# Performance work log

Hardware: AMD Instinct MI355X
Metric: run time of the kernel (lower is better)

## Reference

```python
import jax, jax.numpy as jnp
import numpy as np

NUM_TOKENS = 4096
IN_FEATURES = 4096
OUT_FEATURES = 4096
MAX_PACKED = 4


def setup_inputs() -> dict:
    key = jax.random.key(0)
    k1, k2, k3 = jax.random.split(key, 3)
    x = jax.random.normal(k1, (NUM_TOKENS, IN_FEATURES), dtype=jnp.float32)
    weight_stacked = jax.random.normal(
        k2, (MAX_PACKED, OUT_FEATURES, IN_FEATURES), dtype=jnp.float32) * 0.02
    indices = jax.random.randint(k3, (NUM_TOKENS,), 0, MAX_PACKED, dtype=jnp.int32)
    return {"x": x, "weight_stacked": weight_stacked, "indices": indices}


def reference(x, weight_stacked, indices):
    # apply_swap: outputs[t] = x[t] @ weight_stacked[indices[t]].T
    # Grouped-GEMM expressed as E dense GEMMs with masked combine
    # (E = max_packed is a small static constant).
    E = weight_stacked.shape[0]
    out = jnp.zeros((x.shape[0], weight_stacked.shape[1]), dtype=x.dtype)
    for e in range(E):
        sel = (indices == e)[:, None].astype(x.dtype)  # [T,1]
        out = out + sel * jnp.einsum('ti,oi->to', x, weight_stacked[e])
    return out
```

## Files before the change

### kernel.cpp

```cpp
#include <hip/hip_runtime.h>

#define T 4096
#define K 4096
#define O 4096
#define E 4
#define BK 64
#define MAXT128 35

typedef __attribute__((ext_vector_type(8))) short bf16x8;
typedef __attribute__((ext_vector_type(4))) float f32x4;

__device__ __forceinline__ unsigned short f2bf(float f) {
  unsigned int u = __float_as_uint(f);
  u += 0x7fffu + ((u >> 16) & 1u);
  return (unsigned short)(u >> 16);
}

__global__ void build_meta(const int* __restrict__ idx, int* __restrict__ perm,
                           int* __restrict__ meta, int4* __restrict__ t256,
                           int4* __restrict__ t128, int4* __restrict__ sched) {
  const int wave = threadIdx.x >> 6;
  const int lane = threadIdx.x & 63;
  __shared__ int s_off[E + 1];
  __shared__ int rtE[20], rtP[20], rtC[20];
  __shared__ int r_sh;
  int total = 0;
  for (int t0 = 0; t0 < T; t0 += 64)
    total += __popcll(__ballot(idx[t0 + lane] == wave));
  if (lane == 0) s_off[wave + 1] = total;
  __syncthreads();
  if (threadIdx.x == 0) {
    s_off[0] = 0;
    for (int e = 0; e < E; e++) s_off[e + 1] += s_off[e];
  }
  __syncthreads();
  int base = s_off[wave];
  const unsigned long long below = (1ull << lane) - 1ull;
  for (int t0 = 0; t0 < T; t0 += 64) {
    int e = idx[t0 + lane];
    unsigned long long m = __ballot(e == wave);
    if (e == wave) perm[base + __popcll(m & below)] = t0 + lane;
    base += __popcll(m);
  }
  if (threadIdx.x == 0) {
    int n = 0;
    for (int e = 0; e < E; e++) {
      int s = s_off[e], c = s_off[e + 1] - s;
      for (int ro = 0; ro < c; ro += 256) {
        rtE[n] = e; rtP[n] = s + ro; rtC[n] = (c - ro) < 256 ? (c - ro) : 256; n++;
      }
    }
    r_sh = n;
    meta[0] = n * 16;
    int n1 = 0;
    for (int e = 0; e < E; e++) {
      int s = s_off[e], c = s_off[e + 1] - s;
      for (int ro = 0; ro < c; ro += 128)
        t128[n1++] = make_int4(e, s + ro, (c - ro) < 128 ? (c - ro) : 128, 0);
    }
    for (; n1 < MAXT128; n1++) t128[n1] = make_int4(-1, 0, 0, 0);
  }
  __syncthreads();
  const int r = r_sh;
  for (int i = threadIdx.x; i < 16 * r; i += 256)
    t256[i] = make_int4(rtE[i >> 4], rtP[i >> 4], rtC[i >> 4], (i & 15) * 256);
  {
    const int b = threadIdx.x;
    const int ru = r - 16;
    const int xcd = b & 7, s = b >> 3;
    const int rt_ = 4 * (xcd >> 1) + (s >> 3);
    const int nt_ = 8 * (xcd & 1) + (s & 7);
    sched[b * 3 + 0] = make_int4(rt_ * 16 + nt_, 0, 16, 0);
    int sgi = 1, u0 = b * ru, u1 = u0 + ru;
    while (u0 < u1) {
      int tI = 256 + (u0 >> 4), q0 = u0 & 15;
      int avail = 16 - q0, want = u1 - u0;
      int take = want < avail ? want : avail;
      sched[b * 3 + sgi] = make_int4(tI, q0, take, 0);
      sgi++; u0 += take;
    }
    for (; sgi < 3; sgi++) sched[b * 3 + sgi] = make_int4(-1, 0, 0, 0);
  }
}

__global__ void zero_rem(const int* __restrict__ meta, const int4* __restrict__ t256,
                         const int* __restrict__ perm, float* __restrict__ out) {
  const int ntiles = meta[0];
  const int tI = 256 + (int)blockIdx.x / 16;
  if (tI >= ntiles) return;
  const int4 td = t256[tI];
  const int rt = (blockIdx.x & 15) * 16 + ((int)threadIdx.x >> 4);
  if (rt >= td.z) return;
  float4* p = (float4*)(out + (size_t)perm[td.y + rt] * O + td.w) + (threadIdx.x & 15) * 4;
  const float4 z = {0.f, 0.f, 0.f, 0.f};
  p[0] = z; p[1] = z; p[2] = z; p[3] = z;
}

__global__ void convert_kernel(const float4* __restrict__ w4, const float* __restrict__ x,
                               const int* __restrict__ perm,
                               ushort4* __restrict__ wb4, ushort4* __restrict__ xg4) {
  const size_t NW4 = (size_t)E * O * K / 4;
  const size_t NX4 = (size_t)T * K / 4;
  const size_t stride = (size_t)gridDim.x * blockDim.x;
  for (size_t i = (size_t)blockIdx.x * blockDim.x + threadIdx.x; i < NW4 + NX4; i += stride) {
    if (i < NW4) {
      float4 v = w4[i];
      wb4[i] = make_ushort4(f2bf(v.x), f2bf(v.y), f2bf(v.z), f2bf(v.w));
    } else {
      size_t j = i - NW4;
      int p = (int)(j >> 10);
      int c = (int)(j & 1023);
      float4 v = *((const float4*)(x + (size_t)perm[p] * K) + c);
      xg4[j] = make_ushort4(f2bf(v.x), f2bf(v.y), f2bf(v.z), f2bf(v.w));
    }
  }
}

__global__ __launch_bounds__(512, 2)
void gemm8p(const unsigned short* __restrict__ xg, const unsigned short* __restrict__ wbb,
            const int* __restrict__ perm, const int4* __restrict__ t256,
            const int4* __restrict__ sched, float* __restrict__ out) {
  __shared__ unsigned short lds[65536];
  const int bid = blockIdx.x;
  const int tid = threadIdx.x;
  const int wid = tid >> 6, lane = tid & 63;
  const int wr = wid >> 2, wc = wid & 3;
  const int kc4 = lane >> 4;
  unsigned short* ldsw = &lds[wid * 512];

#define GLL(gp, lp) __builtin_amdgcn_global_load_lds( \
    (const __attribute__((address_space(1))) void*)(gp), \
    (__attribute__((address_space(3))) void*)(lp), 16, 0, 0)
#define STAGE_A(bo, kh, ko) do { \
    GLL(srcA0 + (ko) + (kh) * 32, ldsw + (bo) + (kh) * 8192); \
    GLL(srcA1 + (ko) + (kh) * 32, ldsw + (bo) + (kh) * 8192 + 4096); \
  } while (0)
#define STAGE_B(bo, kh, ko) do { \
    GLL(srcB0 + (ko) + (kh) * 32, ldsw + (bo) + 16384 + (kh) * 8192); \
    GLL(srcB1 + (ko) + (kh) * 32, ldsw + (bo) + 16384 + (kh) * 8192 + 4096); \
  } while (0)
#define LOAD_AF(bo, ks, mh) do { _Pragma("unroll") \
    for (int mi = 0; mi < 4; ++mi) \
      af[mi] = *(const bf16x8*)&lds[(bo) + (ks) * 8192 + aoff[mh][mi]]; } while (0)
#define LOAD_BF(bo, ks) do { _Pragma("unroll") \
    for (int ni = 0; ni < 4; ++ni) \
      bf[ni] = *(const bf16x8*)&lds[(bo) + 16384 + (ks) * 8192 + boff[ni]]; } while (0)
#define MFMA16(mh) do { _Pragma("unroll") \
    for (int mi = 0; mi < 4; ++mi) _Pragma("unroll") \
      for (int ni = 0; ni < 4; ++ni) \
        acc[(mh) * 4 + mi][ni] = __builtin_amdgcn_mfma_f32_16x16x32_bf16( \
            af[mi], bf[ni], acc[(mh) * 4 + mi][ni], 0, 0, 0); } while (0)
#define BAR() do { __builtin_amdgcn_s_barrier(); asm volatile("" ::: "memory"); } while (0)
#define LGKM0() asm volatile("s_waitcnt lgkmcnt(0)" ::: "memory")
#define VM4() asm volatile("s_waitcnt vmcnt(4)" ::: "memory")
#define VM0() asm volatile("s_waitcnt vmcnt(0)" ::: "memory")

#define KTILE(curc, nxtc, koexpr) do { \
    const int ko = (koexpr); \
    LOAD_AF(curc, 0, 0); LOAD_BF(curc, 0); \
    STAGE_A(nxtc, 0, ko); \
    BAR(); LGKM0(); \
    __builtin_amdgcn_s_setprio(1); MFMA16(0); __builtin_amdgcn_s_setprio(0); \
    BAR(); \
    LOAD_AF(curc, 0, 1); \
    STAGE_B(nxtc, 0, ko); \
    BAR(); LGKM0(); \
    __builtin_amdgcn_s_setprio(1); MFMA16(1); __builtin_amdgcn_s_setprio(0); \
    VM4(); BAR(); \
    LOAD_AF(curc, 1, 0); LOAD_BF(curc, 1); \
    STAGE_A(nxtc, 1, ko); \
    BAR(); LGKM0(); \
    __builtin_amdgcn_s_setprio(1); MFMA16(0); __builtin_amdgcn_s_setprio(0); \
    BAR(); \
    LOAD_AF(curc, 1, 1); \
    STAGE_B(nxtc, 1, ko); \
    BAR(); LGKM0(); \
    __builtin_amdgcn_s_setprio(1); MFMA16(1); __builtin_amdgcn_s_setprio(0); \
    VM4(); BAR(); \
  } while (0)

  int aoff[2][4], boff[4];
#pragma unroll
  for (int mh = 0; mh < 2; ++mh)
#pragma unroll
    for (int mi = 0; mi < 4; ++mi) {
      int r = wr * 128 + mh * 64 + mi * 16 + (lane & 15);
      aoff[mh][mi] = (((r >> 1) << 3) + (((((r & 1) << 2) | kc4)) ^ ((r >> 1) & 7))) * 8;
    }
#pragma unroll
  for (int ni = 0; ni < 4; ++ni) {
    int r = wc * 64 + ni * 16 + (lane & 15);
    boff[ni] = (((r >> 1) << 3) + (((((r & 1) << 2) | kc4)) ^ ((r >> 1) & 7))) * 8;
  }

  for (int sg = 0; sg < 3; ++sg) {
    const int4 sd = sched[bid * 3 + sg];
    if (sd.x < 0) break;
    const int4 td = t256[sd.x];
    const int e = td.x, p0 = td.y, rc = td.z, n0 = td.w;
    const int kt0 = sd.y << 2;
    const int nt = sd.z << 2;

    const unsigned short *srcA0, *srcA1, *srcB0, *srcB1;
    {
      const unsigned short* wB = wbb + (size_t)e * O * K + (size_t)n0 * K;
      int s0 = tid, s1 = 512 + tid;
      int b0 = s0 >> 3, v0 = (s0 & 7) ^ (b0 & 7);
      int r0 = b0 * 2 + (v0 >> 2), c0 = v0 & 3;
      int b1 = s1 >> 3, v1 = (s1 & 7) ^ (b1 & 7);
      int r1 = b1 * 2 + (v1 >> 2), c1 = v1 & 3;
      int ra0 = r0 < rc ? r0 : rc - 1;
      int ra1 = r1 < rc ? r1 : rc - 1;
      srcA0 = xg + (size_t)(p0 + ra0) * K + c0 * 8;
      srcA1 = xg + (size_t)(p0 + ra1) * K + c1 * 8;
      srcB0 = wB + (size_t)r0 * K + c0 * 8;
      srcB1 = wB + (size_t)r1 * K + c1 * 8;
    }

    f32x4 acc[8][4] = {};
    bf16x8 af[4], bf[4];

    const int kb = kt0 << 6;
    STAGE_A(0, 0, kb); STAGE_B(0, 0, kb);
    STAGE_A(0, 1, kb); STAGE_B(0, 1, kb);
    VM4(); BAR();

    for (int tp = 0; tp < nt; tp += 2) {
      KTILE(0, 32768, ((tp + 1 < nt ? tp + 1 : tp) + kt0) << 6);
      KTILE(32768, 0, ((tp + 2 < nt ? tp + 2 : tp + 1) + kt0) << 6);
    }
    VM0();

    if (sd.z == 16) {
#pragma unroll
      for (int mh = 0; mh < 2; ++mh)
#pragma unroll
        for (int mi = 0; mi < 4; ++mi) {
          const int rbase = wr * 128 + mh * 64 + mi * 16 + (lane >> 4) * 4;
#pragma unroll
          for (int reg = 0; reg < 4; ++reg) {
            const int pr = rbase + reg;
            if (pr < rc) {
              float* orow = out + (size_t)perm[p0 + pr] * O + n0 + wc * 64 + (lane & 15);
#pragma unroll
              for (int ni = 0; ni < 4; ++ni) orow[ni * 16] = acc[mh * 4 + mi][ni][reg];
            }
          }
        }
    } else {
#pragma unroll
      for (int mh = 0; mh < 2; ++mh)
#pragma unroll
        for (int mi = 0; mi < 4; ++mi) {
          const int rbase = wr * 128 + mh * 64 + mi * 16 + (lane >> 4) * 4;
#pragma unroll
          for (int reg = 0; reg < 4; ++reg) {
            const int pr = rbase + reg;
            if (pr < rc) {
              float* orow = out + (size_t)perm[p0 + pr] * O + n0 + wc * 64 + (lane & 15);
#pragma unroll
              for (int ni = 0; ni < 4; ++ni)
                unsafeAtomicAdd(&orow[ni * 16], acc[mh * 4 + mi][ni][reg]);
            }
          }
        }
    }
  }
}

__global__ __launch_bounds__(256)
void gemm_fb(const float* __restrict__ xf, const float* __restrict__ wf,
             const int* __restrict__ perm, const int4* __restrict__ tiles,
             float* __restrict__ out) {
  __shared__ unsigned short lds_a[128 * 64];
  __shared__ unsigned short lds_b[128 * 64];
  const int4 td = tiles[blockIdx.x];
  if (td.x < 0) return;
  const int e = td.x, p0 = td.y, rc = td.z;
  const int n0 = blockIdx.y * 128;
  const int wave = threadIdx.x >> 6, lane = threadIdx.x & 63;
  const int wr = wave >> 1, wc = wave & 1;
  f32x4 acc[4][4] = {};
  const float* wf_base = wf + (size_t)e * O * K + (size_t)n0 * K;
  for (int k0 = 0; k0 < K; k0 += 64) {
    if (k0) __syncthreads();
#pragma unroll
    for (int i = 0; i < 8; i++) {
      int l4 = i * 256 + (int)threadIdx.x;
      int row = l4 >> 4;
      int c4 = (l4 & 15) << 2;
      int ra = row < rc ? row : (rc - 1);
      const float4 va = *(const float4*)(xf + (size_t)perm[p0 + ra] * K + k0 + c4);
      *(ushort4*)&lds_a[row * 64 + c4] = make_ushort4(f2bf(va.x), f2bf(va.y), f2bf(va.z), f2bf(va.w));
      const float4 vb = *(const float4*)(wf_base + (size_t)row * K + k0 + c4);
      *(ushort4*)&lds_b[row * 64 + c4] = make_ushort4(f2bf(vb.x), f2bf(vb.y), f2bf(vb.z), f2bf(vb.w));
    }
    __syncthreads();
#pragma unroll
    for (int ks = 0; ks < 2; ks++) {
      bf16x8 a2[4], b2[4];
#pragma unroll
      for (int mi = 0; mi < 4; mi++)
        a2[mi] = *(const bf16x8*)&lds_a[(wr * 64 + mi * 16 + (lane & 15)) * 64 + ks * 32 + (lane >> 4) * 8];
#pragma unroll
      for (int ni = 0; ni < 4; ni++)
        b2[ni] = *(const bf16x8*)&lds_b[(wc * 64 + ni * 16 + (lane & 15)) * 64 + ks * 32 + (lane >> 4) * 8];
#pragma unroll
      for (int mi = 0; mi < 4; mi++)
#pragma unroll
        for (int ni = 0; ni < 4; ni++)
          acc[mi][ni] = __builtin_amdgcn_mfma_f32_16x16x32_bf16(a2[mi], b2[ni], acc[mi][ni], 0, 0, 0);
    }
  }
#pragma unroll
  for (int mi = 0; mi < 4; mi++) {
    const int rb = wr * 64 + mi * 16 + (lane >> 4) * 4;
#pragma unroll
    for (int reg = 0; reg < 4; reg++) {
      const int rt = rb + reg;
      if (rt < rc) {
        float* orow = out + (size_t)perm[p0 + rt] * O + n0 + wc * 64 + (lane & 15);
#pragma unroll
        for (int ni = 0; ni < 4; ni++) orow[ni * 16] = acc[mi][ni][reg];
      }
    }
  }
}

extern "C" void kernel_launch(void* const* d_in, const int* in_sizes, int n_in,
                              void* d_out, int out_size, void* d_ws, size_t ws_size,
                              hipStream_t stream) {
  const float* x = (const float*)d_in[0];
  const float* w = (const float*)d_in[1];
  const int* idx = (const int*)d_in[2];
  float* out = (float*)d_out;
  char* ws = (char*)d_ws;

  int* perm = (int*)ws;
  int* meta = (int*)(ws + 16384);
  int4* t256 = (int4*)(ws + 16640);
  int4* t128 = (int4*)(ws + 22528);
  int4* sched = (int4*)(ws + 24576);
  unsigned short* xg = (unsigned short*)(ws + 65536);
  unsigned short* wb = xg + (size_t)T * K;
  const size_t need = 65536 + (size_t)T * K * 2 + (size_t)E * O * K * 2;

  build_meta<<<1, 256, 0, stream>>>(idx, perm, meta, t256, t128, sched);
  if (ws_size >= need) {
    zero_rem<<<768, 256, 0, stream>>>(meta, t256, perm, out);
    convert_kernel<<<2048, 256, 0, stream>>>((const float4*)w, x, perm,
                                             (ushort4*)wb, (ushort4*)xg);
    gemm8p<<<256, 512, 0, stream>>>(xg, wb, perm, t256, sched, out);
  } else {
    gemm_fb<<<dim3(MAXT128, 32), 256, 0, stream>>>(x, w, perm, t128, out);
  }
}
```

Baseline: 276.6 us.

## Double-buffer LDS fragment registers to overlap LDS reads with MFMA

Adds ping-pong register fragment sets (afP/afQ, bfP/bfQ) so the LDS reads for the next MFMA group are issued while the current group computes. This removes the explicit lgkmcnt(0) waits before each MFMA block. It also relaxes the global-load wait to vmcnt(2), adds sched_barriers, and prefetches the first fragments of the next k-tile at the end of the current one. In exchange the kernel uses more VGPRs and the barrier and wait placement changes, so LDS reuse hazards need care.

```diff
diff --git a/kernel.cpp b/kernel.cpp
--- a/kernel.cpp
+++ b/kernel.cpp
@@ -139,44 +139,47 @@
     GLL(srcB0 + (ko) + (kh) * 32, ldsw + (bo) + 16384 + (kh) * 8192); \
     GLL(srcB1 + (ko) + (kh) * 32, ldsw + (bo) + 16384 + (kh) * 8192 + 4096); \
   } while (0)
-#define LOAD_AF(bo, ks, mh) do { _Pragma("unroll") \
+#define LOADA(dst, bo, ks, mh) do { _Pragma("unroll") \
     for (int mi = 0; mi < 4; ++mi) \
-      af[mi] = *(const bf16x8*)&lds[(bo) + (ks) * 8192 + aoff[mh][mi]]; } while (0)
-#define LOAD_BF(bo, ks) do { _Pragma("unroll") \
+      dst[mi] = *(const bf16x8*)&lds[(bo) + (ks) * 8192 + aoff[mh][mi]]; } while (0)
+#define LOADB(dst, bo, ks) do { _Pragma("unroll") \
     for (int ni = 0; ni < 4; ++ni) \
-      bf[ni] = *(const bf16x8*)&lds[(bo) + 16384 + (ks) * 8192 + boff[ni]]; } while (0)
-#define MFMA16(mh) do { _Pragma("unroll") \
+      dst[ni] = *(const bf16x8*)&lds[(bo) + 16384 + (ks) * 8192 + boff[ni]]; } while (0)
+#define MFMA16(A, B, mh) do { _Pragma("unroll") \
     for (int mi = 0; mi < 4; ++mi) _Pragma("unroll") \
       for (int ni = 0; ni < 4; ++ni) \
         acc[(mh) * 4 + mi][ni] = __builtin_amdgcn_mfma_f32_16x16x32_bf16( \
-            af[mi], bf[ni], acc[(mh) * 4 + mi][ni], 0, 0, 0); } while (0)
+            A[mi], B[ni], acc[(mh) * 4 + mi][ni], 0, 0, 0); } while (0)
 #define BAR() do { __builtin_amdgcn_s_barrier(); asm volatile("" ::: "memory"); } while (0)
-#define LGKM0() asm volatile("s_waitcnt lgkmcnt(0)" ::: "memory")
+#define VM2() asm volatile("s_waitcnt vmcnt(2)" ::: "memory")
 #define VM4() asm volatile("s_waitcnt vmcnt(4)" ::: "memory")
 #define VM0() asm volatile("s_waitcnt vmcnt(0)" ::: "memory")
-
-#define KTILE(curc, nxtc, koexpr) do { \
-    const int ko = (koexpr); \
-    LOAD_AF(curc, 0, 0); LOAD_BF(curc, 0); \
-    STAGE_A(nxtc, 0, ko); \
-    BAR(); LGKM0(); \
-    __builtin_amdgcn_s_setprio(1); MFMA16(0); __builtin_amdgcn_s_setprio(0); \
-    BAR(); \
-    LOAD_AF(curc, 0, 1); \
-    STAGE_B(nxtc, 0, ko); \
-    BAR(); LGKM0(); \
-    __builtin_amdgcn_s_setprio(1); MFMA16(1); __builtin_amdgcn_s_setprio(0); \
-    VM4(); BAR(); \
-    LOAD_AF(curc, 1, 0); LOAD_BF(curc, 1); \
-    STAGE_A(nxtc, 1, ko); \
-    BAR(); LGKM0(); \
-    __builtin_amdgcn_s_setprio(1); MFMA16(0); __builtin_amdgcn_s_setprio(0); \
-    BAR(); \
-    LOAD_AF(curc, 1, 1); \
-    STAGE_B(nxtc, 1, ko); \
-    BAR(); LGKM0(); \
-    __builtin_amdgcn_s_setprio(1); MFMA16(1); __builtin_amdgcn_s_setprio(0); \
-    VM4(); BAR(); \
+#define PRIO1() __builtin_amdgcn_s_setprio(1)
+#define PRIO0() __builtin_amdgcn_s_setprio(0)
+#define SCHED0() __builtin_amdgcn_sched_barrier(0)
+
+#define KTILE(C, X, koe) do { \
+    const int ko = (koe); \
+     \
+    LOADA(afQ, C, 0, 1); \
+    STAGE_A(X, 0, ko); \
+    PRIO1(); MFMA16(afP, bfP, 0); PRIO0(); \
+    VM2(); BAR(); SCHED0(); \
+     \
+    LOADA(afP, C, 1, 0); LOADB(bfQ, C, 1); \
+    STAGE_B(X, 0, ko); \
+    PRIO1(); MFMA16(afQ, bfP, 1); PRIO0(); \
+    BAR(); SCHED0(); \
+     \
+    LOADA(afQ, C, 1, 1); \
+    STAGE_A(X, 1, ko); \
+    PRIO1(); MFMA16(afP, bfQ, 0); PRIO0(); \
+    VM2(); BAR(); SCHED0(); \
+     \
+    LOADA(afP, X, 0, 0); LOADB(bfP, X, 0); \
+    STAGE_B(X, 1, ko); \
+    PRIO1(); MFMA16(afQ, bfQ, 1); PRIO0(); \
+    BAR(); SCHED0(); \
   } while (0)
 
   int aoff[2][4], boff[4];
@@ -218,12 +221,13 @@
     }
 
     f32x4 acc[8][4] = {};
-    bf16x8 af[4], bf[4];
+    bf16x8 afP[4], afQ[4], bfP[4], bfQ[4];
 
     const int kb = kt0 << 6;
     STAGE_A(0, 0, kb); STAGE_B(0, 0, kb);
     STAGE_A(0, 1, kb); STAGE_B(0, 1, kb);
     VM4(); BAR();
+    LOADA(afP, 0, 0, 0); LOADB(bfP, 0, 0);
 
     for (int tp = 0; tp < nt; tp += 2) {
       KTILE(0, 32768, ((tp + 1 < nt ? tp + 1 : tp) + kt0) << 6);
```

After: 285.0 us. +3.0%, slower.
